# Performance work log

Measured on AMD Instinct MI355X. Metric: run time of the kernel, lower is better.

Reference implementation:

```python
import jax, jax.numpy as jnp
import numpy as np

N0, N1, N2, N3 = 524288, 262144, 65536, 8192
E0, E1, E2 = 2621440, 655360, 81920
D_IN, D_H, D_OUT = 256, 256, 64


def setup_inputs() -> dict:
    key = jax.random.key(0)
    ks = jax.random.split(key, 16)
    s = 0.02
    inp = {
        "x": jax.random.normal(ks[0], (N0, D_IN), dtype=jnp.float32),
        "src0": jax.random.randint(ks[1], (E0,), 0, N0, dtype=jnp.int32),
        "dst0": jax.random.randint(ks[2], (E0,), 0, N1, dtype=jnp.int32),
        "src1": jax.random.randint(ks[3], (E1,), 0, N1, dtype=jnp.int32),
        "dst1": jax.random.randint(ks[4], (E1,), 0, N2, dtype=jnp.int32),
        "src2": jax.random.randint(ks[5], (E2,), 0, N2, dtype=jnp.int32),
        "dst2": jax.random.randint(ks[6], (E2,), 0, N3, dtype=jnp.int32),
        "nd0": N1, "nd1": N2, "nd2": N3,
        "Wfc": jax.random.normal(ks[7], (D_IN, D_H), dtype=jnp.float32) * s,
        "bfc": jnp.zeros((D_H,), dtype=jnp.float32),
        "Ws0": jax.random.normal(ks[8], (D_H, D_H), dtype=jnp.float32) * s,
        "Wn0": jax.random.normal(ks[9], (D_H, D_H), dtype=jnp.float32) * s,
        "b0": jnp.zeros((D_H,), dtype=jnp.float32),
        "Ws1": jax.random.normal(ks[10], (D_H, D_H), dtype=jnp.float32) * s,
        "Wn1": jax.random.normal(ks[11], (D_H, D_H), dtype=jnp.float32) * s,
        "b1": jnp.zeros((D_H,), dtype=jnp.float32),
        "Ws2": jax.random.normal(ks[12], (D_H, D_OUT), dtype=jnp.float32) * s,
        "Wn2": jax.random.normal(ks[13], (D_H, D_OUT), dtype=jnp.float32) * s,
        "b2": jnp.zeros((D_OUT,), dtype=jnp.float32),
    }
    return inp


def sage_conv(h, src, dst, n_dst, Ws, Wn, b):
    # DGL SAGEConv 'mean': out = h_dst @ W_self + mean_neigh(h_src) @ W_neigh + b
    h_dst = h[:n_dst]
    msg = jnp.take(h, src, axis=0)                    # [E, d] gather
    agg = jax.ops.segment_sum(msg, dst, num_segments=n_dst)
    cnt = jax.ops.segment_sum(jnp.ones((dst.shape[0],), h.dtype), dst, num_segments=n_dst)
    mean = agg / jnp.maximum(cnt, 1.0)[:, None]
    return h_dst @ Ws + mean @ Wn + b


def reference(x, src0, dst0, src1, dst1, src2, dst2, nd0, nd1, nd2,
              Wfc, bfc, Ws0, Wn0, b0, Ws1, Wn1, b1, Ws2, Wn2, b2):
    h = jax.nn.relu(x @ Wfc + bfc)                    # input projection (dropout=0 -> identity)
    h = jax.nn.relu(sage_conv(h, src0, dst0, nd0, Ws0, Wn0, b0))
    h = jax.nn.relu(sage_conv(h, src1, dst1, nd1, Ws1, Wn1, b1))
    h = sage_conv(h, src2, dst2, nd2, Ws2, Wn2, b2)   # no activation on final layer
    return h
```

## Files before the change

kernel.cpp:

```cpp
#include <hip/hip_runtime.h>

constexpr int N0c = 524288, N1c = 262144, N2c = 65536, N3c = 8192;
constexpr int NTOT = N1c + N2c + N3c;

typedef __attribute__((ext_vector_type(8))) short   bf16x8;
typedef __attribute__((ext_vector_type(4))) float   f32x4;
typedef __attribute__((ext_vector_type(8))) unsigned short u16x8;

__device__ inline unsigned short f2bf(float f) {
    union { float f; unsigned u; } v; v.f = f;
    unsigned r = v.u + 0x7FFF + ((v.u >> 16) & 1);
    return (unsigned short)(r >> 16);
}
__device__ inline float bf2f(unsigned short u) {
    union { unsigned u; float f; } v; v.u = ((unsigned)u) << 16;
    return v.f;
}

__device__ inline void glds16(const void* g, void* l) {
    __builtin_amdgcn_global_load_lds(
        (const __attribute__((address_space(1))) unsigned int*)g,
        (__attribute__((address_space(3))) unsigned int*)l, 16, 0, 0);
}

struct WPack { const float* w[7]; unsigned short* o[7]; };

__global__ __launch_bounds__(256)
void wconv_all(WPack p, int* __restrict__ hist)
{
    if (blockIdx.x >= 1408) {
        const int zid = (blockIdx.x - 1408) * 256 + threadIdx.x;
        ((int4*)hist)[zid] = make_int4(0, 0, 0, 0);
        return;
    }
    const int idx = blockIdx.x * 256 + threadIdx.x;
    int widx, off, N;
    if (idx < 327680) { widx = idx >> 16; off = idx & 65535; N = 256; }
    else {
        const int r = idx - 327680;
        widx = 5 + (r >> 14); off = r & 16383; N = 64;
        if (widx > 6) return;
    }
    const int k = off / N, n = off % N;
    p.o[widx][n * 256 + k] = f2bf(p.w[widx][off]);
}

__device__ inline bf16x8 pack_bf8(const float* p) {
    const f32x4 u = *(const f32x4*)p;
    const f32x4 v = *(const f32x4*)(p + 4);
    bf16x8 t;
    #pragma unroll
    for (int j = 0; j < 4; ++j) {
        t[j]     = (short)f2bf(u[j]);
        t[j + 4] = (short)f2bf(v[j]);
    }
    return t;
}

struct CsrArgs {
    const int* src0; const int* dst0;
    const int* src1; const int* dst1;
    const int* src2; const int* dst2;
    int e0, e01, etot;
};

template<int KC>
__device__ inline const unsigned short*
frag_src(const unsigned short* Wt, int r, int kh)
{
    constexpr int SK = KC / 32;
    const int s  = r >> 6;
    const int l  = r & 63;
    const int nt = s / SK;
    const int k0i = s % SK;
    const int n  = nt * 16 + (l & 15);
    const int kg = k0i * 4 + (l >> 4);
    return Wt + n * 256 + kh * KC + kg * 8;
}

template<int NT, int KC, bool DUAL, bool RELU, bool A_F32, bool OUT_BF16>
__device__ inline void gemm_body(const void* A1v, const void* A2v,
                                 const unsigned short* Wt1,
                                 const unsigned short* Wt2,
                                 const float* bias, void* Cv,
                                 unsigned short* Bs, int bid, int t)
{
    constexpr int N    = NT * 16;
    constexpr int PH   = 256 / KC;
    constexpr int SK   = KC / 32;
    constexpr int GPM  = 64 * NT * SK;
    constexpr int TOTG = GPM * (DUAL ? 2 : 1);
    static_assert(TOTG % 1024 == 0, "stage sizing");

    const int lane = t & 63;
    const int wv   = t >> 6;
    const int col  = lane & 15;
    const int kq   = lane >> 4;
    const long row0 = (long)bid * 256 + wv * 16;

    const unsigned short* A1h = (const unsigned short*)A1v;
    const float*          A1f = (const float*)A1v;
    const unsigned short* A2h = (const unsigned short*)A2v;

    f32x4 acc[NT];
    #pragma unroll
    for (int nt = 0; nt < NT; ++nt) acc[nt] = (f32x4){0.f, 0.f, 0.f, 0.f};

    const long ar = (row0 + col) * 256;

    #pragma unroll
    for (int kh = 0; kh < PH; ++kh) {
        if (kh) __syncthreads();
        #pragma unroll
        for (int it = 0; it < TOTG / 1024; ++it) {
            const int g = it * 1024 + t;
            const int m = DUAL ? (g / GPM) : 0;
            const int r = DUAL ? (g % GPM) : g;
            glds16(frag_src<KC>(m ? Wt2 : Wt1, r, kh),
                   &Bs[(it * 1024 + wv * 64) * 8]);
        }
        __syncthreads();

        #pragma unroll
        for (int k0i = 0; k0i < SK; ++k0i) {
            const long ac = ar + kh * KC + k0i * 32 + kq * 8;
            bf16x8 a1, a2;
            if constexpr (A_F32) a1 = pack_bf8(&A1f[ac]);
            else                 a1 = *(const bf16x8*)&A1h[ac];
            if constexpr (DUAL)  a2 = *(const bf16x8*)&A2h[ac];
            #pragma unroll
            for (int nt = 0; nt < NT; ++nt) {
                const bf16x8 b1 = *(const bf16x8*)&Bs[((nt * SK + k0i) * 64 + lane) * 8];
                acc[nt] = __builtin_amdgcn_mfma_f32_16x16x32_bf16(a1, b1, acc[nt], 0, 0, 0);
                if constexpr (DUAL) {
                    const bf16x8 b2 = *(const bf16x8*)&Bs[(GPM + (nt * SK + k0i) * 64 + lane) * 8];
                    acc[nt] = __builtin_amdgcn_mfma_f32_16x16x32_bf16(a2, b2, acc[nt], 0, 0, 0);
                }
            }
        }
    }

    #pragma unroll
    for (int nt = 0; nt < NT; ++nt) {
        const int c = nt * 16 + col;
        const float bb = bias[c];
        #pragma unroll
        for (int rr = 0; rr < 4; ++rr) {
            const long row = row0 + kq * 4 + rr;
            float o = acc[nt][rr] + bb;
            if constexpr (RELU) o = fmaxf(o, 0.f);
            if constexpr (OUT_BF16)
                ((unsigned short*)Cv)[row * N + c] = f2bf(o);
            else
                ((float*)Cv)[row * N + c] = o;
        }
    }
}

__global__ __launch_bounds__(1024, 4)
void fc_rank_k(const float* __restrict__ A1f, const unsigned short* __restrict__ Wt1,
               const float* __restrict__ bias, unsigned short* __restrict__ Cv,
               CsrArgs a, int* __restrict__ hist, int* __restrict__ rank,
               int gemmBlocks)
{
    __shared__ unsigned short Bs[8192 * 8];
    if ((int)blockIdx.x >= gemmBlocks) {
        const int i = ((int)blockIdx.x - gemmBlocks) * 1024 + (int)threadIdx.x;
        if (i >= a.etot) return;
        const int* dstp; int e, hb;
        if (i < a.e0)       { dstp = a.dst0; e = i;         hb = 0; }
        else if (i < a.e01) { dstp = a.dst1; e = i - a.e0;  hb = N1c; }
        else                { dstp = a.dst2; e = i - a.e01; hb = N1c + N2c; }
        rank[i] = atomicAdd(&hist[hb + dstp[e]], 1);
        return;
    }
    gemm_body<16, 256, false, true, true, true>(
        A1f, nullptr, Wt1, nullptr, bias, Cv, Bs, (int)blockIdx.x, (int)threadIdx.x);
}

template<bool RELU, bool OUT_BF16>
__global__ __launch_bounds__(1024, 4)
void gemm_dual_k(const void* __restrict__ A1v, const void* __restrict__ A2v,
                 const unsigned short* __restrict__ Wt1,
                 const unsigned short* __restrict__ Wt2,
                 const float* __restrict__ bias, void* __restrict__ Cv)
{
    __shared__ unsigned short Bs[8192 * 8];
    gemm_body<16, 128, true, RELU, false, OUT_BF16>(
        A1v, A2v, Wt1, Wt2, bias, Cv, Bs, (int)blockIdx.x, (int)threadIdx.x);
}

__global__ __launch_bounds__(1024, 4)
void gemm_fin_k(const void* __restrict__ A1v, const void* __restrict__ A2v,
                const unsigned short* __restrict__ Wt1,
                const unsigned short* __restrict__ Wt2,
                const float* __restrict__ bias, void* __restrict__ Cv)
{
    __shared__ unsigned short Bs[4096 * 8];
    gemm_body<4, 256, true, false, false, false>(
        A1v, A2v, Wt1, Wt2, bias, Cv, Bs, (int)blockIdx.x, (int)threadIdx.x);
}

__global__ __launch_bounds__(256)
void scan1_k(const int* __restrict__ hist, int* __restrict__ offs,
             int* __restrict__ bsum, int n)
{
    __shared__ int sm[256];
    const int t = threadIdx.x;
    const int base = blockIdx.x * 1024 + t * 4;
    int4 v = make_int4(0, 0, 0, 0);
    if (base < n) v = *(const int4*)&hist[base];
    const int s = v.x + v.y + v.z + v.w;
    int val = s;
    sm[t] = val; __syncthreads();
    #pragma unroll
    for (int off = 1; off < 256; off <<= 1) {
        const int add = (t >= off) ? sm[t - off] : 0;
        __syncthreads();
        val += add;
        sm[t] = val;
        __syncthreads();
    }
    const int excl = val - s;
    if (base < n) {
        offs[base]     = excl;
        offs[base + 1] = excl + v.x;
        offs[base + 2] = excl + v.x + v.y;
        offs[base + 3] = excl + v.x + v.y + v.z;
    }
    if (t == 255) bsum[blockIdx.x] = val;
}

__global__ __launch_bounds__(512)
void scan2_k(int* __restrict__ bsum, int nb)
{
    __shared__ int sm[512];
    const int t = threadIdx.x;
    const int s = (t < nb) ? bsum[t] : 0;
    int val = s;
    sm[t] = val; __syncthreads();
    #pragma unroll
    for (int off = 1; off < 512; off <<= 1) {
        const int add = (t >= off) ? sm[t - off] : 0;
        __syncthreads();
        val += add;
        sm[t] = val;
        __syncthreads();
    }
    if (t < nb) bsum[t] = val - s;
}

__global__ __launch_bounds__(256)
void scan3_k(int* __restrict__ offs, const int* __restrict__ bsum, int etot)
{
    const int i = blockIdx.x * 256 + threadIdx.x;
    offs[i] += bsum[i >> 10];
    if (i == 0) offs[NTOT] = etot;
}

__global__ __launch_bounds__(256)
void place_k(CsrArgs a, const int* __restrict__ offs, const int* __restrict__ rank,
             int* __restrict__ ssrc)
{
    const int i = blockIdx.x * 256 + threadIdx.x;
    if (i >= a.etot) return;
    const int* dstp; const int* srcp; int e, hb;
    if (i < a.e0)       { dstp = a.dst0; srcp = a.src0; e = i;         hb = 0; }
    else if (i < a.e01) { dstp = a.dst1; srcp = a.src1; e = i - a.e0;  hb = N1c; }
    else                { dstp = a.dst2; srcp = a.src2; e = i - a.e01; hb = N1c + N2c; }
    const int g = hb + dstp[e];
    ssrc[offs[g] + rank[i]] = srcp[e];
}

__global__ __launch_bounds__(256)
void agg_k(const unsigned short* __restrict__ h, const int* __restrict__ ssrc,
           const int* __restrict__ ob, unsigned short* __restrict__ agg, int n)
{
    const int w    = blockIdx.x * 4 + (threadIdx.x >> 6);
    const int lane = threadIdx.x & 63;
    if (w >= n) return;
    const int beg = ob[w];
    const int end = ob[w + 1];
    const int hf  = lane >> 5;
    const int co  = (lane & 31) * 8;

    float acc[8] = {0.f, 0.f, 0.f, 0.f, 0.f, 0.f, 0.f, 0.f};

    int j = beg;
    for (; j + 16 <= end; j += 16) {
        u16x8 v[8];
        #pragma unroll
        for (int q = 0; q < 8; ++q)
            v[q] = *(const u16x8*)&h[(size_t)ssrc[j + 2 * q + hf] * 256 + co];
        #pragma unroll
        for (int q = 0; q < 8; ++q)
            #pragma unroll
            for (int c = 0; c < 8; ++c) acc[c] += bf2f(v[q][c]);
    }
    const int rem = end - j;
    if (rem > 8) {
        u16x8 v[8]; bool ok[8];
        #pragma unroll
        for (int q = 0; q < 8; ++q) {
            const int e = j + 2 * q + hf;
            ok[q] = (e < end);
            v[q] = *(const u16x8*)&h[(size_t)ssrc[ok[q] ? e : (end - 1)] * 256 + co];
        }
        #pragma unroll
        for (int q = 0; q < 8; ++q)
            #pragma unroll
            for (int c = 0; c < 8; ++c) acc[c] += ok[q] ? bf2f(v[q][c]) : 0.0f;
    } else if (rem > 0) {
        u16x8 v[4]; bool ok[4];
        #pragma unroll
        for (int q = 0; q < 4; ++q) {
            const int e = j + 2 * q + hf;
            ok[q] = (e < end);
            v[q] = *(const u16x8*)&h[(size_t)ssrc[ok[q] ? e : (end - 1)] * 256 + co];
        }
        #pragma unroll
        for (int q = 0; q < 4; ++q)
            #pragma unroll
            for (int c = 0; c < 8; ++c) acc[c] += ok[q] ? bf2f(v[q][c]) : 0.0f;
    }

    #pragma unroll
    for (int c = 0; c < 8; ++c) acc[c] += __shfl_xor(acc[c], 32);

    if (hf == 0) {
        const float inv = 1.0f / fmaxf((float)(end - beg), 1.0f);
        u16x8 o;
        #pragma unroll
        for (int c = 0; c < 8; ++c) o[c] = f2bf(acc[c] * inv);
        *(u16x8*)&agg[(size_t)w * 256 + co] = o;
    }
}

extern "C" void kernel_launch(void* const* d_in, const int* in_sizes, int n_in,
                              void* d_out, int out_size, void* d_ws, size_t ws_size,
                              hipStream_t stream)
{
    const float* x    = (const float*)d_in[0];
    const int*   src0 = (const int*)d_in[1];
    const int*   dst0 = (const int*)d_in[2];
    const int*   src1 = (const int*)d_in[3];
    const int*   dst1 = (const int*)d_in[4];
    const int*   src2 = (const int*)d_in[5];
    const int*   dst2 = (const int*)d_in[6];
    const float* Wfc  = (const float*)d_in[10];
    const float* bfc  = (const float*)d_in[11];
    const float* Ws0  = (const float*)d_in[12];
    const float* Wn0  = (const float*)d_in[13];
    const float* b0   = (const float*)d_in[14];
    const float* Ws1  = (const float*)d_in[15];
    const float* Wn1  = (const float*)d_in[16];
    const float* b1   = (const float*)d_in[17];
    const float* Ws2  = (const float*)d_in[18];
    const float* Wn2  = (const float*)d_in[19];
    const float* b2   = (const float*)d_in[20];
    const int E0 = in_sizes[1], E1 = in_sizes[3], E2 = in_sizes[5];
    const int Etot = E0 + E1 + E2;

    char* ws = (char*)d_ws;
    unsigned short* h0   = (unsigned short*)ws;
    unsigned short* h1   = (unsigned short*)(ws + (256ULL << 20));
    unsigned short* h2   = (unsigned short*)(ws + (384ULL << 20));
    unsigned short* agg  = (unsigned short*)(ws + (416ULL << 20));
    unsigned short* Wt   = (unsigned short*)(ws + (544ULL << 20));
    int*            hist = (int*)(ws + (545ULL << 20));
    int*            offs = (int*)(ws + (547ULL << 20));
    int*            bsum = (int*)(ws + (549ULL << 20));
    int*            ssrc = (int*)(ws + (550ULL << 20));
    int*            rank = (int*)(ws + (564ULL << 20));

    unsigned short* wfc = Wt;
    unsigned short* ws0 = Wt + 65536;
    unsigned short* wn0 = Wt + 131072;
    unsigned short* ws1 = Wt + 196608;
    unsigned short* wn1 = Wt + 262144;
    unsigned short* ws2 = Wt + 327680;
    unsigned short* wn2 = Wt + 344064;

    const dim3 blk(256);

    WPack wp;
    wp.w[0] = Wfc; wp.w[1] = Ws0; wp.w[2] = Wn0; wp.w[3] = Ws1; wp.w[4] = Wn1;
    wp.w[5] = Ws2; wp.w[6] = Wn2;
    wp.o[0] = wfc; wp.o[1] = ws0; wp.o[2] = wn0; wp.o[3] = ws1; wp.o[4] = wn1;
    wp.o[5] = ws2; wp.o[6] = wn2;
    wconv_all<<<dim3(1408 + 328), blk, 0, stream>>>(wp, hist);

    CsrArgs ca;
    ca.src0 = src0; ca.dst0 = dst0; ca.src1 = src1; ca.dst1 = dst1;
    ca.src2 = src2; ca.dst2 = dst2;
    ca.e0 = E0; ca.e01 = E0 + E1; ca.etot = Etot;
    const int gemmBlocks = N0c / 256;
    const int rankBlocks = (Etot + 1023) / 1024;
    fc_rank_k<<<dim3(gemmBlocks + rankBlocks), dim3(1024), 0, stream>>>(
        x, wfc, bfc, h0, ca, hist, rank, gemmBlocks);

    scan1_k<<<dim3(NTOT / 1024), blk, 0, stream>>>(hist, offs, bsum, NTOT);
    scan2_k<<<dim3(1), dim3(512), 0, stream>>>(bsum, NTOT / 1024);
    scan3_k<<<dim3(NTOT / 256), blk, 0, stream>>>(offs, bsum, Etot);
    place_k<<<dim3((Etot + 255) / 256), blk, 0, stream>>>(ca, offs, rank, ssrc);

    agg_k<<<dim3(N1c / 4), blk, 0, stream>>>(h0, ssrc, offs, agg, N1c);
    gemm_dual_k<true, true><<<dim3(N1c / 256), dim3(1024), 0, stream>>>(
        h0, agg, ws0, wn0, b0, h1);

    agg_k<<<dim3(N2c / 4), blk, 0, stream>>>(h1, ssrc, offs + N1c, agg, N2c);
    gemm_dual_k<true, true><<<dim3(N2c / 256), dim3(1024), 0, stream>>>(
        h1, agg, ws1, wn1, b1, h2);

    agg_k<<<dim3(N3c / 4), blk, 0, stream>>>(h2, ssrc, offs + N1c + N2c, agg, N3c);
    gemm_fin_k<<<dim3(N3c / 256), dim3(1024), 0, stream>>>(
        h2, agg, ws2, wn2, b2, (float*)d_out);
}
```

Baseline: 870.3 us.

## Halve GEMM block size and prefetch A fragments into registers across k-phases

```diff
diff --git a/kernel.cpp b/kernel.cpp
--- a/kernel.cpp
+++ b/kernel.cpp
@@ -45,9 +45,7 @@
     p.o[widx][n * 256 + k] = f2bf(p.w[widx][off]);
 }
 
-__device__ inline bf16x8 pack_bf8(const float* p) {
-    const f32x4 u = *(const f32x4*)p;
-    const f32x4 v = *(const f32x4*)(p + 4);
+__device__ inline bf16x8 pack_pair(const f32x4 u, const f32x4 v) {
     bf16x8 t;
     #pragma unroll
     for (int j = 0; j < 4; ++j) {
@@ -90,13 +88,13 @@
     constexpr int SK   = KC / 32;
     constexpr int GPM  = 64 * NT * SK;
     constexpr int TOTG = GPM * (DUAL ? 2 : 1);
-    static_assert(TOTG % 1024 == 0, "stage sizing");
+    static_assert(TOTG % 512 == 0, "stage sizing");
 
     const int lane = t & 63;
     const int wv   = t >> 6;
     const int col  = lane & 15;
     const int kq   = lane >> 4;
-    const long row0 = (long)bid * 256 + wv * 16;
+    const long row0 = (long)bid * 128 + wv * 16;
 
     const unsigned short* A1h = (const unsigned short*)A1v;
     const float*          A1f = (const float*)A1v;
@@ -108,26 +106,39 @@
 
     const long ar = (row0 + col) * 256;
 
-    #pragma unroll
-    for (int kh = 0; kh < PH; ++kh) {
-        if (kh) __syncthreads();
-        #pragma unroll
-        for (int it = 0; it < TOTG / 1024; ++it) {
-            const int g = it * 1024 + t;
+    f32x4  fbuf[2][SK][2];
+    bf16x8 h1buf[2][SK], h2buf[2][SK];
+
+    auto issue_a = [&](int kh, int b) {
+        #pragma unroll
+        for (int q = 0; q < SK; ++q) {
+            const long ac = ar + kh * KC + q * 32 + kq * 8;
+            if constexpr (A_F32) {
+                fbuf[b][q][0] = *(const f32x4*)&A1f[ac];
+                fbuf[b][q][1] = *(const f32x4*)&A1f[ac + 4];
+            } else {
+                h1buf[b][q] = *(const bf16x8*)&A1h[ac];
+                if constexpr (DUAL) h2buf[b][q] = *(const bf16x8*)&A2h[ac];
+            }
+        }
+    };
+    auto stage_w = [&](int kh) {
+        #pragma unroll
+        for (int it = 0; it < TOTG / 512; ++it) {
+            const int g = it * 512 + t;
             const int m = DUAL ? (g / GPM) : 0;
             const int r = DUAL ? (g % GPM) : g;
             glds16(frag_src<KC>(m ? Wt2 : Wt1, r, kh),
-                   &Bs[(it * 1024 + wv * 64) * 8]);
-        }
-        __syncthreads();
-
+                   &Bs[(it * 512 + wv * 64) * 8]);
+        }
+    };
+    auto compute = [&](int b) {
         #pragma unroll
         for (int k0i = 0; k0i < SK; ++k0i) {
-            const long ac = ar + kh * KC + k0i * 32 + kq * 8;
             bf16x8 a1, a2;
-            if constexpr (A_F32) a1 = pack_bf8(&A1f[ac]);
-            else                 a1 = *(const bf16x8*)&A1h[ac];
-            if constexpr (DUAL)  a2 = *(const bf16x8*)&A2h[ac];
+            if constexpr (A_F32) a1 = pack_pair(fbuf[b][k0i][0], fbuf[b][k0i][1]);
+            else                 a1 = h1buf[b][k0i];
+            if constexpr (DUAL)  a2 = h2buf[b][k0i];
             #pragma unroll
             for (int nt = 0; nt < NT; ++nt) {
                 const bf16x8 b1 = *(const bf16x8*)&Bs[((nt * SK + k0i) * 64 + lane) * 8];
@@ -138,6 +149,21 @@
                 }
             }
         }
+    };
+
+    issue_a(0, 0);
+    stage_w(0);
+    __syncthreads();
+
+    #pragma unroll
+    for (int kh = 0; kh < PH; ++kh) {
+        if (kh + 1 < PH) issue_a(kh + 1, (kh + 1) & 1);
+        compute(kh & 1);
+        if (kh + 1 < PH) {
+            __syncthreads();
+            stage_w(kh + 1);
+            __syncthreads();
+        }
     }
 
     #pragma unroll
@@ -157,15 +183,15 @@
     }
 }
 
-__global__ __launch_bounds__(1024, 4)
+__global__ __launch_bounds__(512, 4)
 void fc_rank_k(const float* __restrict__ A1f, const unsigned short* __restrict__ Wt1,
                const float* __restrict__ bias, unsigned short* __restrict__ Cv,
                CsrArgs a, int* __restrict__ hist, int* __restrict__ rank,
                int gemmBlocks)
 {
-    __shared__ unsigned short Bs[8192 * 8];
+    __shared__ unsigned short Bs[4096 * 8];
     if ((int)blockIdx.x >= gemmBlocks) {
-        const int i = ((int)blockIdx.x - gemmBlocks) * 1024 + (int)threadIdx.x;
+        const int i = ((int)blockIdx.x - gemmBlocks) * 512 + (int)threadIdx.x;
         if (i >= a.etot) return;
         const int* dstp; int e, hb;
         if (i < a.e0)       { dstp = a.dst0; e = i;         hb = 0; }
@@ -174,30 +200,30 @@
         rank[i] = atomicAdd(&hist[hb + dstp[e]], 1);
         return;
     }
-    gemm_body<16, 256, false, true, true, true>(
+    gemm_body<16, 128, false, true, true, true>(
         A1f, nullptr, Wt1, nullptr, bias, Cv, Bs, (int)blockIdx.x, (int)threadIdx.x);
 }
 
 template<bool RELU, bool OUT_BF16>
-__global__ __launch_bounds__(1024, 4)
+__global__ __launch_bounds__(512, 4)
 void gemm_dual_k(const void* __restrict__ A1v, const void* __restrict__ A2v,
                  const unsigned short* __restrict__ Wt1,
                  const unsigned short* __restrict__ Wt2,
                  const float* __restrict__ bias, void* __restrict__ Cv)
 {
-    __shared__ unsigned short Bs[8192 * 8];
-    gemm_body<16, 128, true, RELU, false, OUT_BF16>(
+    __shared__ unsigned short Bs[4096 * 8];
+    gemm_body<16, 64, true, RELU, OUT_BF16 && false, OUT_BF16>(
         A1v, A2v, Wt1, Wt2, bias, Cv, Bs, (int)blockIdx.x, (int)threadIdx.x);
 }
 
-__global__ __launch_bounds__(1024, 4)
+__global__ __launch_bounds__(512, 4)
 void gemm_fin_k(const void* __restrict__ A1v, const void* __restrict__ A2v,
                 const unsigned short* __restrict__ Wt1,
                 const unsigned short* __restrict__ Wt2,
                 const float* __restrict__ bias, void* __restrict__ Cv)
 {
-    __shared__ unsigned short Bs[4096 * 8];
-    gemm_body<4, 256, true, false, false, false>(
+    __shared__ unsigned short Bs[2048 * 8];
+    gemm_body<4, 128, true, false, false, false>(
         A1v, A2v, Wt1, Wt2, bias, Cv, Bs, (int)blockIdx.x, (int)threadIdx.x);
 }
 
@@ -394,9 +420,9 @@
     ca.src0 = src0; ca.dst0 = dst0; ca.src1 = src1; ca.dst1 = dst1;
     ca.src2 = src2; ca.dst2 = dst2;
     ca.e0 = E0; ca.e01 = E0 + E1; ca.etot = Etot;
-    const int gemmBlocks = N0c / 256;
-    const int rankBlocks = (Etot + 1023) / 1024;
-    fc_rank_k<<<dim3(gemmBlocks + rankBlocks), dim3(1024), 0, stream>>>(
+    const int gemmBlocks = N0c / 128;
+    const int rankBlocks = (Etot + 511) / 512;
+    fc_rank_k<<<dim3(gemmBlocks + rankBlocks), dim3(512), 0, stream>>>(
         x, wfc, bfc, h0, ca, hist, rank, gemmBlocks);
 
     scan1_k<<<dim3(NTOT / 1024), blk, 0, stream>>>(hist, offs, bsum, NTOT);
@@ -405,14 +431,14 @@
     place_k<<<dim3((Etot + 255) / 256), blk, 0, stream>>>(ca, offs, rank, ssrc);
 
     agg_k<<<dim3(N1c / 4), blk, 0, stream>>>(h0, ssrc, offs, agg, N1c);
-    gemm_dual_k<true, true><<<dim3(N1c / 256), dim3(1024), 0, stream>>>(
+    gemm_dual_k<true, true><<<dim3(N1c / 128), dim3(512), 0, stream>>>(
         h0, agg, ws0, wn0, b0, h1);
 
     agg_k<<<dim3(N2c / 4), blk, 0, stream>>>(h1, ssrc, offs + N1c, agg, N2c);
-    gemm_dual_k<true, true><<<dim3(N2c / 256), dim3(1024), 0, stream>>>(
+    gemm_dual_k<true, true><<<dim3(N2c / 128), dim3(512), 0, stream>>>(
         h1, agg, ws1, wn1, b1, h2);
 
     agg_k<<<dim3(N3c / 4), blk, 0, stream>>>(h2, ssrc, offs + N1c + N2c, agg, N3c);
-    gemm_fin_k<<<dim3(N3c / 256), dim3(1024), 0, stream>>>(
+    gemm_fin_k<<<dim3(N3c / 128), dim3(512), 0, stream>>>(
         h2, agg, ws2, wn2, b2, (float*)d_out);
 }
```

New measurement: 863.2 us. About the same (-0.8%).
